# Kernel tuning notes

Hardware: AMD Instinct MI355X
Metric: run time of the kernel (lower is better)

The kernel has to match this reference:

```python
import jax, jax.numpy as jnp
import numpy as np
from jax import lax

B, T, F, H, D = 16384, 79, 3, 256, 256  # batch, levels, n_input_fields, rnn_channels, dense_width


def setup_inputs() -> dict:
    key = jax.random.key(0)
    ks = jax.random.split(key, 8)
    return {
        "x0": jax.random.normal(ks[0], (B, T), dtype=jnp.float32),
        "x1": jax.random.normal(ks[1], (B, T), dtype=jnp.float32),
        "x2": jax.random.normal(ks[2], (B, T), dtype=jnp.float32),
        # SimpleRNN params: kernel [F,H], recurrent kernel [H,H] (scaled small so relu recurrence stays stable), bias [H]
        "W_in": jax.random.normal(ks[3], (F, H), dtype=jnp.float32) * 0.1,
        "U": jax.random.normal(ks[4], (H, H), dtype=jnp.float32) * 0.05,
        "b_rnn": jnp.zeros((H,), dtype=jnp.float32),
        # MLPBlock depth=1: single Dense(D)
        "W_d": jax.random.normal(ks[5], (H, D), dtype=jnp.float32) * 0.05,
        "b_d": jnp.zeros((D,), dtype=jnp.float32),
    }


def reference(x0, x1, x2, W_in, U, b_rnn, W_d, b_d):
    # CombineInputs(-1, expand=True): stack fields on new trailing axis -> [B, T, F]
    x = jnp.stack([x0, x1, x2], axis=-1)
    # go_backwards=True: SimpleRNN consumes the sequence in reverse order
    x = x[:, ::-1, :]
    # Batched input projection (hoisted out of the recurrence): [B, T, H]
    xp = jnp.einsum("btf,fh->bth", x, W_in) + b_rnn
    xp_t = jnp.swapaxes(xp, 0, 1)  # [T, B, H] for scan over time

    def step(h, xt):
        h = jax.nn.relu(xt + h @ U)
        return h, None

    h0 = jnp.zeros((x.shape[0], W_in.shape[1]), dtype=x.dtype)
    hT, _ = lax.scan(step, h0, xp_t)  # final hidden state [B, H]
    # MLPBlock(depth=1, combine_inputs=False): single Dense, no activation
    return hT @ W_d + b_d
```

## Files before the change

kernel.cpp:

```cpp
#include <hip/hip_runtime.h>
#include <hip/hip_bf16.h>
#include <stdint.h>

#define Bsz   16384
#define Tt    79
#define Hh    256
#define Dd    256
#define KP    272
#define LROW  280
#define NTILE 32
#define THR   256

typedef __attribute__((ext_vector_type(8)))  short  short8;
typedef __attribute__((ext_vector_type(4)))  float  float4_;
typedef __attribute__((ext_vector_type(16))) float  float16_;

__device__ __forceinline__ unsigned short f2bf(float f){
  unsigned u = __float_as_uint(f);
  u += 0x7fffu + ((u >> 16) & 1u);
  return (unsigned short)(u >> 16);
}
__device__ __forceinline__ unsigned pk2(float a, float b){
  unsigned r;
  asm("v_cvt_pk_bf16_f32 %0, %1, %2" : "=v"(r) : "v"(a), "v"(b));
  return r;
}

__global__ void build_tables(const float* __restrict__ W_in,
                             const float* __restrict__ U,
                             const float* __restrict__ b_rnn,
                             const float* __restrict__ W_d,
                             const float* __restrict__ b_d,
                             unsigned short* __restrict__ Ut,
                             unsigned short* __restrict__ Wdt){
  const int TBL = 256 * KP;
  int idx = blockIdx.x * 256 + threadIdx.x;
  if (idx >= 2 * TBL) return;
  int tb  = idx / TBL;
  int rem = idx - tb * TBL;
  int m = rem / KP;
  int k = rem - m * KP;
  float v = 0.f;
  if (tb == 0){
    if      (k < 256) v = U[k * 256 + m];
    else if (k < 259) v = W_in[(k - 256) * 256 + m];
    else if (k == 259) v = b_rnn[m];
  } else {
    if      (k < 256) v = W_d[k * 256 + m];
    else if (k == 259) v = b_d[m];
  }
  unsigned short o = f2bf(v);
  if (tb == 0) Ut[rem] = o; else Wdt[rem] = o;
}

__global__ __launch_bounds__(THR, 2) void rnn_main(
    const float* __restrict__ x0,
    const float* __restrict__ x1,
    const float* __restrict__ x2,
    const unsigned short* __restrict__ Ut,
    const unsigned short* __restrict__ Wdt,
    float* __restrict__ out){
  __shared__ __align__(16) short hbuf[2][NTILE * LROW];

  const int tid  = threadIdx.x;
  const int lane = tid & 63;
  const int wm   = tid >> 6;
  const int nrow = lane & 31;
  const int hi   = lane >> 5;
  const int hi8  = hi * 8;
  const int hi4  = hi * 4;
  const int bbase = blockIdx.x * NTILE;

  {
    int4* p = (int4*)&hbuf[0][0];
    const int tot = 2 * NTILE * LROW * 2 / 16;
    int4 z = make_int4(0, 0, 0, 0);
    for (int i = tid; i < tot; i += THR) p[i] = z;
  }
  __syncthreads();

  if (tid < NTILE){
    hbuf[0][tid * LROW + 259] = (short)0x3F80;
    hbuf[1][tid * LROW + 259] = (short)0x3F80;
  }

  const bool stager = (wm == 0) && (lane < NTILE);
  const int  sn  = lane & (NTILE - 1);
  const int  sgb = bbase + sn;
  if (stager){
    int tr = Tt - 1;
    float a = x0[sgb * Tt + tr];
    float b = x1[sgb * Tt + tr];
    float c = x2[sgb * Tt + tr];
    *(unsigned*)&hbuf[0][sn * LROW + 256] = pk2(a, b);
    hbuf[0][sn * LROW + 258] = (short)f2bf(c);
  }

  short8 afr[2][17];
  #pragma unroll
  for (int mt = 0; mt < 2; ++mt){
    const unsigned short* p = Ut + (wm * 64 + mt * 32 + nrow) * KP + hi8;
    #pragma unroll
    for (int kt = 0; kt < 17; ++kt){
      afr[mt][kt] = *(const short8*)(p + kt * 16);
    }
  }

  __syncthreads();

  const float16_ zz = {0.f,0.f,0.f,0.f,0.f,0.f,0.f,0.f,
                       0.f,0.f,0.f,0.f,0.f,0.f,0.f,0.f};
  float16_ acc[2];

  #pragma unroll 1
  for (int t = 0; t < Tt; ++t){
    float xa = 0.f, xb = 0.f, xc = 0.f;
    if (stager && t < Tt - 1){
      int tr = Tt - 2 - t;
      xa = x0[sgb * Tt + tr];
      xb = x1[sgb * Tt + tr];
      xc = x2[sgb * Tt + tr];
    }

    const short* hb = &hbuf[t & 1][0];
    short*       hw = &hbuf[(t + 1) & 1][0];
    const short* rbase = &hb[nrow * LROW + hi8];

    __builtin_amdgcn_s_setprio(1);
    #pragma unroll
    for (int kt = 0; kt < 17; ++kt){
      short8 b = *(const short8*)(rbase + kt * 16);
      if (kt == 0){
        acc[0] = __builtin_amdgcn_mfma_f32_32x32x16_bf16(afr[0][0], b, zz, 0, 0, 0);
        acc[1] = __builtin_amdgcn_mfma_f32_32x32x16_bf16(afr[1][0], b, zz, 0, 0, 0);
      } else {
        acc[0] = __builtin_amdgcn_mfma_f32_32x32x16_bf16(afr[0][kt], b, acc[0], 0, 0, 0);
        acc[1] = __builtin_amdgcn_mfma_f32_32x32x16_bf16(afr[1][kt], b, acc[1], 0, 0, 0);
      }
    }
    __builtin_amdgcn_s_setprio(0);

    #pragma unroll
    for (int mt = 0; mt < 2; ++mt){
      #pragma unroll
      for (int q = 0; q < 4; ++q){
        uint2 w;
        w.x = pk2(fmaxf(acc[mt][4*q+0], 0.f), fmaxf(acc[mt][4*q+1], 0.f));
        w.y = pk2(fmaxf(acc[mt][4*q+2], 0.f), fmaxf(acc[mt][4*q+3], 0.f));
        *(uint2*)&hw[nrow * LROW + wm * 64 + mt * 32 + 8 * q + hi4] = w;
      }
    }
    if (stager && t < Tt - 1){
      *(unsigned*)&hw[sn * LROW + 256] = pk2(xa, xb);
      hw[sn * LROW + 258] = (short)f2bf(xc);
    }

    __syncthreads();
  }

  const short* hb = &hbuf[Tt & 1][0];
  float16_ oacc[2];
  #pragma unroll
  for (int kt = 0; kt < 17; ++kt){
    short8 b  = *(const short8*)&hb[nrow * LROW + kt * 16 + hi8];
    short8 w0 = *(const short8*)(Wdt + (wm * 64 +  0 + nrow) * KP + kt * 16 + hi8);
    short8 w1 = *(const short8*)(Wdt + (wm * 64 + 32 + nrow) * KP + kt * 16 + hi8);
    if (kt == 0){
      oacc[0] = __builtin_amdgcn_mfma_f32_32x32x16_bf16(w0, b, zz, 0, 0, 0);
      oacc[1] = __builtin_amdgcn_mfma_f32_32x32x16_bf16(w1, b, zz, 0, 0, 0);
    } else {
      oacc[0] = __builtin_amdgcn_mfma_f32_32x32x16_bf16(w0, b, oacc[0], 0, 0, 0);
      oacc[1] = __builtin_amdgcn_mfma_f32_32x32x16_bf16(w1, b, oacc[1], 0, 0, 0);
    }
  }

  #pragma unroll
  for (int mt = 0; mt < 2; ++mt){
    #pragma unroll
    for (int q = 0; q < 4; ++q){
      float4_ v = {oacc[mt][4*q+0], oacc[mt][4*q+1],
                   oacc[mt][4*q+2], oacc[mt][4*q+3]};
      *(float4_*)&out[(bbase + nrow) * Dd + wm * 64 + mt * 32 + 8 * q + hi4] = v;
    }
  }
}

extern "C" void kernel_launch(void* const* d_in, const int* in_sizes, int n_in,
                              void* d_out, int out_size, void* d_ws, size_t ws_size,
                              hipStream_t stream){
  const float* x0    = (const float*)d_in[0];
  const float* x1    = (const float*)d_in[1];
  const float* x2    = (const float*)d_in[2];
  const float* W_in  = (const float*)d_in[3];
  const float* U     = (const float*)d_in[4];
  const float* b_rnn = (const float*)d_in[5];
  const float* W_d   = (const float*)d_in[6];
  const float* b_d   = (const float*)d_in[7];

  unsigned short* Ut  = (unsigned short*)d_ws;
  unsigned short* Wdt = Ut + 256 * KP;
  float* out = (float*)d_out;

  build_tables<<<(2 * 256 * KP + 255) / 256, 256, 0, stream>>>(W_in, U, b_rnn, W_d, b_d, Ut, Wdt);
  rnn_main<<<Bsz / NTILE, THR, 0, stream>>>(x0, x1, x2, Ut, Wdt, out);
}
```

Measured before the change: 210.4 us.

## Overlap barrier wait with wave-local k-tiles of the recurrence matmul

Each wave now rotates its k-tile order so it starts with the four k-tiles of the hidden state that it wrote itself in the previous step. Those tiles need no barrier, so they are issued before the __syncthreads and the remaining thirteen come after it. The barrier moves from the end of each step to the middle, with one final barrier after the loop. The goal is to hide barrier wait and skew between waves behind MFMA work, at the cost of a 17-entry offset table and per-wave rotated fragment ordering.

```diff
diff --git a/kernel.cpp b/kernel.cpp
--- a/kernel.cpp
+++ b/kernel.cpp
@@ -96,13 +96,20 @@
     hbuf[0][sn * LROW + 258] = (short)f2bf(c);
   }
 
+  int offB[17];
+  #pragma unroll
+  for (int j = 0; j < 17; ++j){
+    int ktg = 4 * wm + j; if (ktg >= 17) ktg -= 17;
+    offB[j] = ktg * 16;
+  }
+
   short8 afr[2][17];
   #pragma unroll
   for (int mt = 0; mt < 2; ++mt){
     const unsigned short* p = Ut + (wm * 64 + mt * 32 + nrow) * KP + hi8;
     #pragma unroll
-    for (int kt = 0; kt < 17; ++kt){
-      afr[mt][kt] = *(const short8*)(p + kt * 16);
+    for (int j = 0; j < 17; ++j){
+      afr[mt][j] = *(const short8*)(p + offB[j]);
     }
   }
 
@@ -114,6 +121,27 @@
 
   #pragma unroll 1
   for (int t = 0; t < Tt; ++t){
+    const short* hb = &hbuf[t & 1][0];
+    short*       hw = &hbuf[(t + 1) & 1][0];
+    const short* rbase = &hb[nrow * LROW + hi8];
+    const short* pA    = rbase + wm * 64;
+
+    __builtin_amdgcn_s_setprio(1);
+    #pragma unroll
+    for (int j = 0; j < 4; ++j){
+      short8 b = *(const short8*)(pA + j * 16);
+      if (j == 0){
+        acc[0] = __builtin_amdgcn_mfma_f32_32x32x16_bf16(afr[0][0], b, zz, 0, 0, 0);
+        acc[1] = __builtin_amdgcn_mfma_f32_32x32x16_bf16(afr[1][0], b, zz, 0, 0, 0);
+      } else {
+        acc[0] = __builtin_amdgcn_mfma_f32_32x32x16_bf16(afr[0][j], b, acc[0], 0, 0, 0);
+        acc[1] = __builtin_amdgcn_mfma_f32_32x32x16_bf16(afr[1][j], b, acc[1], 0, 0, 0);
+      }
+    }
+    __builtin_amdgcn_s_setprio(0);
+
+    __syncthreads();
+
     float xa = 0.f, xb = 0.f, xc = 0.f;
     if (stager && t < Tt - 1){
       int tr = Tt - 2 - t;
@@ -122,21 +150,12 @@
       xc = x2[sgb * Tt + tr];
     }
 
-    const short* hb = &hbuf[t & 1][0];
-    short*       hw = &hbuf[(t + 1) & 1][0];
-    const short* rbase = &hb[nrow * LROW + hi8];
-
     __builtin_amdgcn_s_setprio(1);
     #pragma unroll
-    for (int kt = 0; kt < 17; ++kt){
-      short8 b = *(const short8*)(rbase + kt * 16);
-      if (kt == 0){
-        acc[0] = __builtin_amdgcn_mfma_f32_32x32x16_bf16(afr[0][0], b, zz, 0, 0, 0);
-        acc[1] = __builtin_amdgcn_mfma_f32_32x32x16_bf16(afr[1][0], b, zz, 0, 0, 0);
-      } else {
-        acc[0] = __builtin_amdgcn_mfma_f32_32x32x16_bf16(afr[0][kt], b, acc[0], 0, 0, 0);
-        acc[1] = __builtin_amdgcn_mfma_f32_32x32x16_bf16(afr[1][kt], b, acc[1], 0, 0, 0);
-      }
+    for (int j = 4; j < 17; ++j){
+      short8 b = *(const short8*)(rbase + offB[j]);
+      acc[0] = __builtin_amdgcn_mfma_f32_32x32x16_bf16(afr[0][j], b, acc[0], 0, 0, 0);
+      acc[1] = __builtin_amdgcn_mfma_f32_32x32x16_bf16(afr[1][j], b, acc[1], 0, 0, 0);
     }
     __builtin_amdgcn_s_setprio(0);
 
@@ -154,9 +173,9 @@
       *(unsigned*)&hw[sn * LROW + 256] = pk2(xa, xb);
       hw[sn * LROW + 258] = (short)f2bf(xc);
     }
-
-    __syncthreads();
-  }
+  }
+
+  __syncthreads();
 
   const short* hb = &hbuf[Tt & 1][0];
   float16_ oacc[2];
```

New measurement: 215.6 us. +2.5%, slower.

## Interleave two batch tiles per block to overlap MFMA with epilogue

Applied to the files above, without the earlier changes.

Each block now processes two 32-row batch tiles, 64 rows in total, with separate hidden-state buffers. The second tile's MFMA chain is interleaved with the first tile's ReLU/pack/LDS-store epilogue, and sched_group_barrier pins the instruction mix so matrix work hides the epilogue latency. Each wave's U fragments in registers are now reused across twice as many rows. Occupancy drops to one block per CU, and an LDS padding array is added, apparently to enforce that, which trades inter-block latency hiding for explicit intra-wave overlap.

```diff
diff --git a/kernel.cpp b/kernel.cpp
--- a/kernel.cpp
+++ b/kernel.cpp
@@ -25,6 +25,9 @@
   asm("v_cvt_pk_bf16_f32 %0, %1, %2" : "=v"(r) : "v"(a), "v"(b));
   return r;
 }
+
+#define MFMA32(A,B,C) __builtin_amdgcn_mfma_f32_32x32x16_bf16((A),(B),(C),0,0,0)
+#define SGB(m,n) __builtin_amdgcn_sched_group_barrier((m),(n),0)
 
 __global__ void build_tables(const float* __restrict__ W_in,
                              const float* __restrict__ U,
@@ -53,14 +56,15 @@
   if (tb == 0) Ut[rem] = o; else Wdt[rem] = o;
 }
 
-__global__ __launch_bounds__(THR, 2) void rnn_main(
+__global__ __launch_bounds__(THR, 1) void rnn_main(
     const float* __restrict__ x0,
     const float* __restrict__ x1,
     const float* __restrict__ x2,
     const unsigned short* __restrict__ Ut,
     const unsigned short* __restrict__ Wdt,
     float* __restrict__ out){
-  __shared__ __align__(16) short hbuf[2][NTILE * LROW];
+  __shared__ __align__(16) short hbuf[2][2][NTILE * LROW];
+  __shared__ float ldspad[2700];
 
   const int tid  = threadIdx.x;
   const int lane = tid & 63;
@@ -69,31 +73,35 @@
   const int hi   = lane >> 5;
   const int hi8  = hi * 8;
   const int hi4  = hi * 4;
-  const int bbase = blockIdx.x * NTILE;
+  const int bbase = blockIdx.x * (2 * NTILE);
+
+  asm volatile("" :: "v"((unsigned)(size_t)(void*)ldspad));
 
   {
-    int4* p = (int4*)&hbuf[0][0];
-    const int tot = 2 * NTILE * LROW * 2 / 16;
+    int4* p = (int4*)&hbuf[0][0][0];
+    const int tot = 2 * 2 * NTILE * LROW * 2 / 16;
     int4 z = make_int4(0, 0, 0, 0);
     for (int i = tid; i < tot; i += THR) p[i] = z;
   }
   __syncthreads();
 
   if (tid < NTILE){
-    hbuf[0][tid * LROW + 259] = (short)0x3F80;
-    hbuf[1][tid * LROW + 259] = (short)0x3F80;
-  }
-
-  const bool stager = (wm == 0) && (lane < NTILE);
+    hbuf[0][0][tid * LROW + 259] = (short)0x3F80;
+    hbuf[0][1][tid * LROW + 259] = (short)0x3F80;
+    hbuf[1][0][tid * LROW + 259] = (short)0x3F80;
+    hbuf[1][1][tid * LROW + 259] = (short)0x3F80;
+  }
+
+  const bool stager = (wm < 2) && (lane < NTILE);
   const int  sn  = lane & (NTILE - 1);
-  const int  sgb = bbase + sn;
+  const int  sgb = bbase + wm * NTILE + sn;
   if (stager){
     int tr = Tt - 1;
     float a = x0[sgb * Tt + tr];
     float b = x1[sgb * Tt + tr];
     float c = x2[sgb * Tt + tr];
-    *(unsigned*)&hbuf[0][sn * LROW + 256] = pk2(a, b);
-    hbuf[0][sn * LROW + 258] = (short)f2bf(c);
+    *(unsigned*)&hbuf[0][wm][sn * LROW + 256] = pk2(a, b);
+    hbuf[0][wm][sn * LROW + 258] = (short)f2bf(c);
   }
 
   short8 afr[2][17];
@@ -110,10 +118,16 @@
 
   const float16_ zz = {0.f,0.f,0.f,0.f,0.f,0.f,0.f,0.f,
                        0.f,0.f,0.f,0.f,0.f,0.f,0.f,0.f};
-  float16_ acc[2];
+  float16_ accP[2], accQ[2];
 
   #pragma unroll 1
   for (int t = 0; t < Tt; ++t){
+    const int cb = t & 1, nb = (t + 1) & 1;
+    const short* rbaseP = &hbuf[cb][0][nrow * LROW + hi8];
+    const short* rbaseQ = &hbuf[cb][1][nrow * LROW + hi8];
+    short* hwP = &hbuf[nb][0][0];
+    short* hwQ = &hbuf[nb][1][0];
+
     float xa = 0.f, xb = 0.f, xc = 0.f;
     if (stager && t < Tt - 1){
       int tr = Tt - 2 - t;
@@ -122,22 +136,37 @@
       xc = x2[sgb * Tt + tr];
     }
 
-    const short* hb = &hbuf[t & 1][0];
-    short*       hw = &hbuf[(t + 1) & 1][0];
-    const short* rbase = &hb[nrow * LROW + hi8];
-
     __builtin_amdgcn_s_setprio(1);
     #pragma unroll
     for (int kt = 0; kt < 17; ++kt){
-      short8 b = *(const short8*)(rbase + kt * 16);
+      short8 b = *(const short8*)(rbaseP + kt * 16);
       if (kt == 0){
-        acc[0] = __builtin_amdgcn_mfma_f32_32x32x16_bf16(afr[0][0], b, zz, 0, 0, 0);
-        acc[1] = __builtin_amdgcn_mfma_f32_32x32x16_bf16(afr[1][0], b, zz, 0, 0, 0);
+        accP[0] = MFMA32(afr[0][0], b, zz);
+        accP[1] = MFMA32(afr[1][0], b, zz);
       } else {
-        acc[0] = __builtin_amdgcn_mfma_f32_32x32x16_bf16(afr[0][kt], b, acc[0], 0, 0, 0);
-        acc[1] = __builtin_amdgcn_mfma_f32_32x32x16_bf16(afr[1][kt], b, acc[1], 0, 0, 0);
-      }
-    }
+        accP[0] = MFMA32(afr[0][kt], b, accP[0]);
+        accP[1] = MFMA32(afr[1][kt], b, accP[1]);
+      }
+    }
+
+#define QSTEP(kt) { short8 b = *(const short8*)(rbaseQ + (kt) * 16);           \
+      accQ[0] = MFMA32(afr[0][kt], b, (kt) == 0 ? zz : accQ[0]);               \
+      accQ[1] = MFMA32(afr[1][kt], b, (kt) == 0 ? zz : accQ[1]); }
+#define TAILP(mt,q) { uint2 w;                                                 \
+      w.x = pk2(fmaxf(accP[mt][4*(q)+0], 0.f), fmaxf(accP[mt][4*(q)+1], 0.f)); \
+      w.y = pk2(fmaxf(accP[mt][4*(q)+2], 0.f), fmaxf(accP[mt][4*(q)+3], 0.f)); \
+      *(uint2*)&hwP[nrow * LROW + wm * 64 + (mt) * 32 + 8 * (q) + hi4] = w; }
+#define PIN() { SGB(0x100, 2); SGB(0x8, 4); SGB(0x2, 6); SGB(0x200, 1); }
+
+    QSTEP(0)  QSTEP(1)  TAILP(0,0) PIN()
+    QSTEP(2)  QSTEP(3)  TAILP(0,1) PIN()
+    QSTEP(4)  QSTEP(5)  TAILP(0,2) PIN()
+    QSTEP(6)  QSTEP(7)  TAILP(0,3) PIN()
+    QSTEP(8)  QSTEP(9)  TAILP(1,0) PIN()
+    QSTEP(10) QSTEP(11) TAILP(1,1) PIN()
+    QSTEP(12) QSTEP(13) TAILP(1,2) PIN()
+    QSTEP(14) QSTEP(15) TAILP(1,3) PIN()
+    QSTEP(16)
     __builtin_amdgcn_s_setprio(0);
 
     #pragma unroll
@@ -145,42 +174,47 @@
       #pragma unroll
       for (int q = 0; q < 4; ++q){
         uint2 w;
-        w.x = pk2(fmaxf(acc[mt][4*q+0], 0.f), fmaxf(acc[mt][4*q+1], 0.f));
-        w.y = pk2(fmaxf(acc[mt][4*q+2], 0.f), fmaxf(acc[mt][4*q+3], 0.f));
-        *(uint2*)&hw[nrow * LROW + wm * 64 + mt * 32 + 8 * q + hi4] = w;
-      }
-    }
+        w.x = pk2(fmaxf(accQ[mt][4*q+0], 0.f), fmaxf(accQ[mt][4*q+1], 0.f));
+        w.y = pk2(fmaxf(accQ[mt][4*q+2], 0.f), fmaxf(accQ[mt][4*q+3], 0.f));
+        *(uint2*)&hwQ[nrow * LROW + wm * 64 + mt * 32 + 8 * q + hi4] = w;
+      }
+    }
+
     if (stager && t < Tt - 1){
-      *(unsigned*)&hw[sn * LROW + 256] = pk2(xa, xb);
-      hw[sn * LROW + 258] = (short)f2bf(xc);
+      short* hwS = (wm == 0) ? hwP : hwQ;
+      *(unsigned*)&hwS[sn * LROW + 256] = pk2(xa, xb);
+      hwS[sn * LROW + 258] = (short)f2bf(xc);
     }
 
     __syncthreads();
   }
 
-  const short* hb = &hbuf[Tt & 1][0];
-  float16_ oacc[2];
-  #pragma unroll
-  for (int kt = 0; kt < 17; ++kt){
-    short8 b  = *(const short8*)&hb[nrow * LROW + kt * 16 + hi8];
-    short8 w0 = *(const short8*)(Wdt + (wm * 64 +  0 + nrow) * KP + kt * 16 + hi8);
-    short8 w1 = *(const short8*)(Wdt + (wm * 64 + 32 + nrow) * KP + kt * 16 + hi8);
-    if (kt == 0){
-      oacc[0] = __builtin_amdgcn_mfma_f32_32x32x16_bf16(w0, b, zz, 0, 0, 0);
-      oacc[1] = __builtin_amdgcn_mfma_f32_32x32x16_bf16(w1, b, zz, 0, 0, 0);
-    } else {
-      oacc[0] = __builtin_amdgcn_mfma_f32_32x32x16_bf16(w0, b, oacc[0], 0, 0, 0);
-      oacc[1] = __builtin_amdgcn_mfma_f32_32x32x16_bf16(w1, b, oacc[1], 0, 0, 0);
-    }
-  }
-
-  #pragma unroll
-  for (int mt = 0; mt < 2; ++mt){
-    #pragma unroll
-    for (int q = 0; q < 4; ++q){
-      float4_ v = {oacc[mt][4*q+0], oacc[mt][4*q+1],
-                   oacc[mt][4*q+2], oacc[mt][4*q+3]};
-      *(float4_*)&out[(bbase + nrow) * Dd + wm * 64 + mt * 32 + 8 * q + hi4] = v;
+  #pragma unroll 1
+  for (int tile = 0; tile < 2; ++tile){
+    const short* hb = &hbuf[Tt & 1][tile][0];
+    float16_ oacc[2];
+    #pragma unroll
+    for (int kt = 0; kt < 17; ++kt){
+      short8 b  = *(const short8*)&hb[nrow * LROW + kt * 16 + hi8];
+      short8 w0 = *(const short8*)(Wdt + (wm * 64 +  0 + nrow) * KP + kt * 16 + hi8);
+      short8 w1 = *(const short8*)(Wdt + (wm * 64 + 32 + nrow) * KP + kt * 16 + hi8);
+      if (kt == 0){
+        oacc[0] = MFMA32(w0, b, zz);
+        oacc[1] = MFMA32(w1, b, zz);
+      } else {
+        oacc[0] = MFMA32(w0, b, oacc[0]);
+        oacc[1] = MFMA32(w1, b, oacc[1]);
+      }
+    }
+    const int rowb = bbase + tile * NTILE + nrow;
+    #pragma unroll
+    for (int mt = 0; mt < 2; ++mt){
+      #pragma unroll
+      for (int q = 0; q < 4; ++q){
+        float4_ v = {oacc[mt][4*q+0], oacc[mt][4*q+1],
+                     oacc[mt][4*q+2], oacc[mt][4*q+3]};
+        *(float4_*)&out[rowb * Dd + wm * 64 + mt * 32 + 8 * q + hi4] = v;
+      }
     }
   }
 }
@@ -202,5 +236,5 @@
   float* out = (float*)d_out;
 
   build_tables<<<(2 * 256 * KP + 255) / 256, 256, 0, stream>>>(W_in, U, b_rnn, W_d, b_d, Ut, Wdt);
-  rnn_main<<<Bsz / NTILE, THR, 0, stream>>>(x0, x1, x2, Ut, Wdt, out);
-}
+  rnn_main<<<Bsz / (2 * NTILE), THR, 0, stream>>>(x0, x1, x2, Ut, Wdt, out);
+}
```

Result: slower. 232.5 us (+10.5%).
